# Kernel tuning notes

Hardware: AMD Instinct MI355X
Metric: run time of the kernel (lower is better)

Reference implementation:

```python
import jax, jax.numpy as jnp
import numpy as np

E, D, H, K = 8, 2048, 1024, 2  # num_experts, input_size, hidden_size, top_k
B, L = 2, 1024


def setup_inputs() -> dict:
    key = jax.random.key(0)
    k1, k2, k3, k4 = jax.random.split(key, 4)
    x = jax.random.normal(k1, (B, L, D), dtype=jnp.float32)
    w_gate = jax.random.normal(k2, (E, D), dtype=jnp.float32) * 0.02   # router Linear weight [E, D]
    w_in = jax.random.normal(k3, (E, 2 * H, D), dtype=jnp.float32) * 0.02  # ParallelExperts [E, out=2H, in=D]
    w_out = jax.random.normal(k4, (E, D, H), dtype=jnp.float32) * 0.02     # ParallelExperts [E, out=D, in=H]
    bias = jnp.zeros((D,), dtype=jnp.float32)
    return {"x": x, "w_gate": w_gate, "w_in": w_in, "w_out": w_out, "bias": bias}


def _moe_forward(x, w_gate, w_in, w_out, bias):
    bsz, length, d = x.shape
    xt = x.reshape(-1, d)  # [T, D]
    # top-k router: logits -> top-k -> softmax over selected logits
    logits = xt @ w_gate.T  # [T, E]
    topk_vals, topk_idx = jax.lax.top_k(logits, K)  # [T, K]
    topk_gates = jax.nn.softmax(topk_vals, axis=-1)  # [T, K]
    T = xt.shape[0]
    # dense [T, E] gate matrix; zero for non-selected experts, so the dense
    # per-expert compute below is mathematically identical to gathered dispatch
    gates = jnp.zeros((T, E), dtype=xt.dtype).at[jnp.arange(T)[:, None], topk_idx].add(topk_gates)
    # expert GLU FFN, vectorized over experts
    h = jnp.einsum('td,efd->tef', xt, w_in)  # [T, E, 2H]
    h1, h2 = jnp.split(h, 2, axis=-1)
    a = jax.nn.silu(h1) * h2                 # [T, E, H]
    eo = jnp.einsum('teh,edh->ted', a, w_out)  # [T, E, D]
    y = jnp.einsum('ted,te->td', eo, gates) + bias
    return y.reshape(bsz, length, d)


def reference(x, w_gate, w_in, w_out, bias):
    y = _moe_forward(x, w_gate, w_in, w_out, bias)
    loss = jnp.float32(0.0)  # router aux loss is 0 in eval mode (JetMoE top_k_gating)
    return (y, loss)
```

## Files before the change

### kernel.cpp

```cpp
#include <hip/hip_runtime.h>

#define E_    8
#define D_    2048
#define H_    1024
#define T_    2048
#define BK    64

using u16   = unsigned short;
using s16x8 = __attribute__((ext_vector_type(8))) short;
using f32x4 = __attribute__((ext_vector_type(4))) float;

__device__ __forceinline__ u16 f2bf(float f) {
  union { float f; unsigned u; } v; v.f = f;
  unsigned r = v.u + 0x7fffu + ((v.u >> 16) & 1u);
  return (u16)(r >> 16);
}
__device__ __forceinline__ s16x8 cvt8(f32x4 a, f32x4 b) {
  s16x8 o;
  o[0]=(short)f2bf(a.x); o[1]=(short)f2bf(a.y); o[2]=(short)f2bf(a.z); o[3]=(short)f2bf(a.w);
  o[4]=(short)f2bf(b.x); o[5]=(short)f2bf(b.y); o[6]=(short)f2bf(b.z); o[7]=(short)f2bf(b.w);
  return o;
}
__device__ __forceinline__ int slot(int r, int c) { return r * 64 + ((c ^ (r & 7)) << 3); }


__global__ __launch_bounds__(256) void init_kernel(
    const float* __restrict__ bias, float* __restrict__ out, int* __restrict__ counts)
{
  int idx = blockIdx.x * 256 + threadIdx.x;
  if (blockIdx.x == 0 && threadIdx.x < E_) counts[threadIdx.x] = 0;
  if (idx == 0) out[(size_t)T_ * D_] = 0.0f;
  int dq = idx & (D_ / 4 - 1);
  f32x4 b = *(const f32x4*)(bias + dq * 4);
  *(f32x4*)(out + (size_t)idx * 4) = b;
}

__global__ __launch_bounds__(256) void router_kernel(
    const float* __restrict__ x, const float* __restrict__ wg,
    u16* __restrict__ xb, int* __restrict__ lists, float* __restrict__ gates,
    int* __restrict__ counts)
{
  int t = blockIdx.x;
  int tid = threadIdx.x;
  const float* xr = x + (size_t)t * D_;
  float acc[E_];
#pragma unroll
  for (int e = 0; e < E_; ++e) acc[e] = 0.f;
#pragma unroll
  for (int i = 0; i < D_ / 256; ++i) {
    int d = tid + 256 * i;
    float xv = xr[d];
    xb[(size_t)t * D_ + d] = f2bf(xv);
#pragma unroll
    for (int e = 0; e < E_; ++e) acc[e] += xv * wg[e * D_ + d];
  }
#pragma unroll
  for (int off = 32; off >= 1; off >>= 1)
#pragma unroll
    for (int e = 0; e < E_; ++e) acc[e] += __shfl_down(acc[e], off);

  __shared__ float red[4][E_];
  int w = tid >> 6, lane = tid & 63;
  if (lane == 0)
#pragma unroll
    for (int e = 0; e < E_; ++e) red[w][e] = acc[e];
  __syncthreads();
  if (tid == 0) {
    float v0 = -1e30f, v1 = -1e30f; int e0 = 0, e1 = 0;
#pragma unroll
    for (int e = 0; e < E_; ++e) {
      float v = red[0][e] + red[1][e] + red[2][e] + red[3][e];
      if (v > v0)      { v1 = v0; e1 = e0; v0 = v; e0 = e; }
      else if (v > v1) { v1 = v;  e1 = e; }
    }
    float g1 = expf(v1 - v0);
    float inv = 1.f / (1.f + g1);
    float g0 = inv; g1 *= inv;
    int s0 = atomicAdd(&counts[e0], 1);
    lists[e0 * T_ + s0] = t * 2 + 0;
    gates[t * 2 + 0] = g0;
    int s1 = atomicAdd(&counts[e1], 1);
    lists[e1 * T_ + s1] = t * 2 + 1;
    gates[t * 2 + 1] = g1;
  }
}

__global__ __launch_bounds__(512) void gemm1_kernel(
    const u16* __restrict__ xb, const float* __restrict__ w_in,
    const int* __restrict__ lists, const int* __restrict__ counts,
    u16* __restrict__ a_buf)
{
  int e = blockIdx.z, bm = blockIdx.y, bn = blockIdx.x;
  int Ne = counts[e];
  if (bm * 256 >= Ne) return;

  __shared__ __align__(16) u16 As[2][256 * 64];
  __shared__ __align__(16) u16 Bs[2][128 * 64];

  int tid = threadIdx.x, w = tid >> 6, lane = tid & 63;
  int sr = tid >> 3, sc = tid & 7;
  int br = tid >> 2, bc = (tid & 3) * 2;

  const u16* aptr[4];
#pragma unroll
  for (int i = 0; i < 4; ++i) {
    int gr = bm * 256 + sr + 64 * i;
    aptr[i] = (gr < Ne) ? (xb + (size_t)(lists[e * T_ + gr] >> 1) * D_ + sc * 8) : nullptr;
  }
  int o = bn * 64 + ((br >> 5) & 1) * H_ + (br >> 6) * 32 + (br & 31);
  const float* bptr = w_in + (size_t)e * (2 * H_) * D_ + (size_t)o * D_ + bc * 8;

  s16x8 areg[4]; f32x4 bl[4];
#define LOADS1(K) { _Pragma("unroll") for (int i = 0; i < 4; ++i) { \
                      s16x8 v = {0,0,0,0,0,0,0,0}; \
                      if (aptr[i]) v = *(const s16x8*)(aptr[i] + (K)); areg[i] = v; } \
                    _Pragma("unroll") for (int i = 0; i < 4; ++i) \
                      bl[i] = *(const f32x4*)(bptr + (K) + i * 4); }
#define STAGE1(B) { _Pragma("unroll") for (int i = 0; i < 4; ++i) \
                      *(s16x8*)(&As[B][slot(sr + 64 * i, sc)]) = areg[i]; \
                    *(s16x8*)(&Bs[B][slot(br, bc)])     = cvt8(bl[0], bl[1]); \
                    *(s16x8*)(&Bs[B][slot(br, bc + 1)]) = cvt8(bl[2], bl[3]); }

  f32x4 acc[4][4];
#pragma unroll
  for (int m = 0; m < 4; ++m)
#pragma unroll
    for (int n = 0; n < 4; ++n) acc[m][n] = (f32x4){0.f, 0.f, 0.f, 0.f};

  int wr = (w >> 1) * 64, wc = (w & 1) * 64, lrow = lane & 15, g = lane >> 4;

  LOADS1(0);
  STAGE1(0);
  __syncthreads();
  const int NT = D_ / BK;
  for (int kt = 0; kt < NT; ++kt) {
    int cur = kt & 1;
    if (kt + 1 < NT) LOADS1((kt + 1) * BK);
#pragma unroll
    for (int ks = 0; ks < 2; ++ks) {
      int ch = ks * 4 + g;
      s16x8 af[4], bf[4];
#pragma unroll
      for (int m = 0; m < 4; ++m) af[m] = *(const s16x8*)(&As[cur][slot(wr + m * 16 + lrow, ch)]);
#pragma unroll
      for (int n = 0; n < 4; ++n) bf[n] = *(const s16x8*)(&Bs[cur][slot(wc + n * 16 + lrow, ch)]);
#pragma unroll
      for (int m = 0; m < 4; ++m)
#pragma unroll
        for (int n = 0; n < 4; ++n)
          acc[m][n] = __builtin_amdgcn_mfma_f32_16x16x32_bf16(af[m], bf[n], acc[m][n], 0, 0, 0);
    }
    if (kt + 1 < NT) {
      STAGE1(cur ^ 1);
      __syncthreads();
    }
  }
  int lcol = lane & 15, lr4 = (lane >> 4) * 4;
  int wcc = (w & 1) * 32;
#pragma unroll
  for (int m = 0; m < 4; ++m)
#pragma unroll
    for (int q = 0; q < 4; ++q) {
      int row = bm * 256 + wr + m * 16 + lr4 + q;
      if (row < Ne) {
#pragma unroll
        for (int n = 0; n < 2; ++n) {
          float h1 = acc[m][n][q], h2 = acc[m][n + 2][q];
          float a = (h1 / (1.f + __expf(-h1))) * h2;
          a_buf[((size_t)e * T_ + row) * H_ + bn * 64 + wcc + n * 16 + lcol] = f2bf(a);
        }
      }
    }
}

__global__ __launch_bounds__(512) void gemm2_kernel(
    const u16* __restrict__ a_buf, const float* __restrict__ w_out,
    const int* __restrict__ lists, const int* __restrict__ counts,
    const float* __restrict__ gates, float* __restrict__ out)
{
  int e = blockIdx.z, bm = blockIdx.y, bn = blockIdx.x;
  int Ne = counts[e];
  if (bm * 256 >= Ne) return;

  __shared__ __align__(16) u16 As[2][256 * 64];
  __shared__ __align__(16) u16 Bs[2][128 * 64];

  int tid = threadIdx.x, w = tid >> 6, lane = tid & 63;
  int sr = tid >> 3, sc = tid & 7;
  int br = tid >> 2, bc = (tid & 3) * 2;

  const u16* aptr[4];
#pragma unroll
  for (int i = 0; i < 4; ++i) {
    int gr = bm * 256 + sr + 64 * i;
    aptr[i] = (gr < Ne) ? (a_buf + ((size_t)e * T_ + gr) * H_ + sc * 8) : nullptr;
  }
  const float* bptr = w_out + (size_t)e * D_ * H_ + (size_t)(bn * 128 + br) * H_ + bc * 8;

  s16x8 areg[4]; f32x4 bl[4];
#define LOADS2(K) { _Pragma("unroll") for (int i = 0; i < 4; ++i) { \
                      s16x8 v = {0,0,0,0,0,0,0,0}; \
                      if (aptr[i]) v = *(const s16x8*)(aptr[i] + (K)); areg[i] = v; } \
                    _Pragma("unroll") for (int i = 0; i < 4; ++i) \
                      bl[i] = *(const f32x4*)(bptr + (K) + i * 4); }
#define STAGE2(B) { _Pragma("unroll") for (int i = 0; i < 4; ++i) \
                      *(s16x8*)(&As[B][slot(sr + 64 * i, sc)]) = areg[i]; \
                    *(s16x8*)(&Bs[B][slot(br, bc)])     = cvt8(bl[0], bl[1]); \
                    *(s16x8*)(&Bs[B][slot(br, bc + 1)]) = cvt8(bl[2], bl[3]); }

  f32x4 acc[4][4];
#pragma unroll
  for (int m = 0; m < 4; ++m)
#pragma unroll
    for (int n = 0; n < 4; ++n) acc[m][n] = (f32x4){0.f, 0.f, 0.f, 0.f};

  int wr = (w >> 1) * 64, wc = (w & 1) * 64, lrow = lane & 15, g = lane >> 4;

  LOADS2(0);
  STAGE2(0);
  __syncthreads();
  const int NT = H_ / BK;
  for (int kt = 0; kt < NT; ++kt) {
    int cur = kt & 1;
    if (kt + 1 < NT) LOADS2((kt + 1) * BK);
#pragma unroll
    for (int ks = 0; ks < 2; ++ks) {
      int ch = ks * 4 + g;
      s16x8 af[4], bf[4];
#pragma unroll
      for (int m = 0; m < 4; ++m) af[m] = *(const s16x8*)(&As[cur][slot(wr + m * 16 + lrow, ch)]);
#pragma unroll
      for (int n = 0; n < 4; ++n) bf[n] = *(const s16x8*)(&Bs[cur][slot(wc + n * 16 + lrow, ch)]);
#pragma unroll
      for (int m = 0; m < 4; ++m)
#pragma unroll
        for (int n = 0; n < 4; ++n)
          acc[m][n] = __builtin_amdgcn_mfma_f32_16x16x32_bf16(af[m], bf[n], acc[m][n], 0, 0, 0);
    }
    if (kt + 1 < NT) {
      STAGE2(cur ^ 1);
      __syncthreads();
    }
  }
  int lcol = lane & 15, lr4 = (lane >> 4) * 4;
#pragma unroll
  for (int m = 0; m < 4; ++m)
#pragma unroll
    for (int q = 0; q < 4; ++q) {
      int row = bm * 256 + wr + m * 16 + lr4 + q;
      if (row < Ne) {
        int p = lists[e * T_ + row];
        float gt = gates[p];
        int t = p >> 1;
#pragma unroll
        for (int n = 0; n < 4; ++n)
          atomicAdd(&out[(size_t)t * D_ + bn * 128 + wc + n * 16 + lcol], gt * acc[m][n][q]);
      }
    }
}

extern "C" void kernel_launch(void* const* d_in, const int* in_sizes, int n_in,
                              void* d_out, int out_size, void* d_ws, size_t ws_size,
                              hipStream_t stream)
{
  const float* x      = (const float*)d_in[0];
  const float* w_gate = (const float*)d_in[1];
  const float* w_in   = (const float*)d_in[2];
  const float* w_out  = (const float*)d_in[3];
  const float* bias   = (const float*)d_in[4];
  float* out = (float*)d_out;

  char* ws = (char*)d_ws;
  u16*   xb     = (u16*)(ws);
  u16*   a_buf  = (u16*)(ws + 8388608);
  int*   lists  = (int*)(ws + 41943040);
  float* gates  = (float*)(ws + 42008576);
  int*   counts = (int*)(ws + 42024960);

  init_kernel<<<T_ * D_ / 4 / 256, 256, 0, stream>>>(bias, out, counts);
  router_kernel<<<T_, 256, 0, stream>>>(x, w_gate, xb, lists, gates, counts);
  dim3 g1(H_ / 64, 8, E_);
  gemm1_kernel<<<g1, 512, 0, stream>>>(xb, w_in, lists, counts, a_buf);
  dim3 g2(D_ / 128, 8, E_);
  gemm2_kernel<<<g2, 512, 0, stream>>>(a_buf, w_out, lists, counts, gates, out);
}
```

Before: 232.5 us.

## Use persistent grid-stride tile scheduling with narrower N tiles and direct-to-LDS loads

Both grouped GEMMs now launch a fixed grid of 512 blocks. Each block walks a flattened list of (expert M-tile, N-tile) work items through a prefix scan over per-expert counts, so no blocks launch only to exit early. The N tile is halved to 64 and occupancy is hinted at 4 blocks per CU. Activation tiles go straight into LDS via global_load_lds with a pre-swizzled column, replacing the register staging. Narrower tiles cut per-tile reuse of the gathered activations and double the number of tiles, and out-of-range rows are now clamped to the last valid row instead of zeroed.

```diff
diff --git a/kernel.cpp b/kernel.cpp
--- a/kernel.cpp
+++ b/kernel.cpp
@@ -5,6 +5,7 @@
 #define H_    1024
 #define T_    2048
 #define BK    64
+#define NN    32
 
 using u16   = unsigned short;
 using s16x8 = __attribute__((ext_vector_type(8))) short;
@@ -22,6 +23,20 @@
   return o;
 }
 __device__ __forceinline__ int slot(int r, int c) { return r * 64 + ((c ^ (r & 7)) << 3); }
+
+__device__ __forceinline__ void gload16(const void* g, void* l) {
+  __builtin_amdgcn_global_load_lds((const __attribute__((address_space(1))) void*)g,
+                                   (__attribute__((address_space(3))) void*)l, 16, 0, 0);
+}
+
+#define FIND_EXPERT(ml, cnt, e, mt, Ne)                        \
+  { int b_ = 0;                                                \
+    _Pragma("unroll")                                          \
+    for (int i_ = 0; i_ < E_; ++i_) {                          \
+      int ti_ = (cnt[i_] + 255) >> 8;                          \
+      if ((ml) >= b_ && (ml) < b_ + ti_) {                     \
+        e = i_; mt = (ml) - b_; Ne = cnt[i_]; }                \
+      b_ += ti_; } }
 
 
 __global__ __launch_bounds__(256) void init_kernel(
@@ -85,178 +100,186 @@
   }
 }
 
-__global__ __launch_bounds__(512) void gemm1_kernel(
+__global__ __launch_bounds__(512, 4) void gemm1_kernel(
     const u16* __restrict__ xb, const float* __restrict__ w_in,
     const int* __restrict__ lists, const int* __restrict__ counts,
     u16* __restrict__ a_buf)
 {
-  int e = blockIdx.z, bm = blockIdx.y, bn = blockIdx.x;
-  int Ne = counts[e];
-  if (bm * 256 >= Ne) return;
-
   __shared__ __align__(16) u16 As[2][256 * 64];
-  __shared__ __align__(16) u16 Bs[2][128 * 64];
+  __shared__ __align__(16) u16 Bs[2][64 * 64];
+
+  int cnt[E_];
+#pragma unroll
+  for (int i = 0; i < E_; ++i) cnt[i] = counts[i];
+  int mt_total = 0;
+#pragma unroll
+  for (int i = 0; i < E_; ++i) mt_total += (cnt[i] + 255) >> 8;
+  int total = mt_total * NN;
 
   int tid = threadIdx.x, w = tid >> 6, lane = tid & 63;
-  int sr = tid >> 3, sc = tid & 7;
-  int br = tid >> 2, bc = (tid & 3) * 2;
-
-  const u16* aptr[4];
-#pragma unroll
-  for (int i = 0; i < 4; ++i) {
-    int gr = bm * 256 + sr + 64 * i;
-    aptr[i] = (gr < Ne) ? (xb + (size_t)(lists[e * T_ + gr] >> 1) * D_ + sc * 8) : nullptr;
+  int swzc = ((lane & 7) ^ (lane >> 3)) * 8;
+  int brow = tid >> 3, bch = tid & 7;
+  int wr = (w >> 1) * 64, wcB = (w & 1) * 32, lrow = lane & 15, g = lane >> 4;
+  int lcol = lane & 15, lr4 = (lane >> 4) * 4;
+
+  int bswz = (blockIdx.x & 7) * 64 + (blockIdx.x >> 3);
+
+  for (int t = bswz; t < total; t += 512) {
+    int ml = t >> 5, n = t & (NN - 1);
+    int e = 0, mt = 0, Ne = 0;
+    FIND_EXPERT(ml, cnt, e, mt, Ne);
+
+    const u16* ap[4];
+#pragma unroll
+    for (int i = 0; i < 4; ++i) {
+      int gr = mt * 256 + 32 * w + 8 * i + (lane >> 3);
+      if (gr >= Ne) gr = Ne - 1;
+      ap[i] = xb + (size_t)(lists[e * T_ + gr] >> 1) * D_ + swzc;
+    }
+    int o = n * 32 + ((brow >> 4) & 1) * H_ + (brow >> 5) * 16 + (brow & 15);
+    const float* bp = w_in + (size_t)e * (2 * H_) * D_ + (size_t)o * D_ + bch * 8;
+
+    f32x4 acc[4][2];
+#pragma unroll
+    for (int m = 0; m < 4; ++m) { acc[m][0] = (f32x4){0,0,0,0}; acc[m][1] = (f32x4){0,0,0,0}; }
+
+    f32x4 bl0 = *(const f32x4*)(bp), bl1 = *(const f32x4*)(bp + 4);
+#pragma unroll
+    for (int i = 0; i < 4; ++i) gload16(ap[i], &As[0][(32 * w + 8 * i) * 64]);
+    *(s16x8*)(&Bs[0][slot(brow, bch)]) = cvt8(bl0, bl1);
+    __syncthreads();
+
+    const int NT = D_ / BK;
+    for (int kt = 0; kt < NT; ++kt) {
+      int cur = kt & 1;
+      if (kt + 1 < NT) {
+        int k = (kt + 1) * BK;
+        bl0 = *(const f32x4*)(bp + k); bl1 = *(const f32x4*)(bp + k + 4);
+#pragma unroll
+        for (int i = 0; i < 4; ++i) gload16(ap[i] + k, &As[cur ^ 1][(32 * w + 8 * i) * 64]);
+      }
+#pragma unroll
+      for (int ks = 0; ks < 2; ++ks) {
+        int ch = ks * 4 + g;
+        s16x8 af[4], bf[2];
+#pragma unroll
+        for (int m = 0; m < 4; ++m) af[m] = *(const s16x8*)(&As[cur][slot(wr + m * 16 + lrow, ch)]);
+#pragma unroll
+        for (int nn = 0; nn < 2; ++nn) bf[nn] = *(const s16x8*)(&Bs[cur][slot(wcB + nn * 16 + lrow, ch)]);
+#pragma unroll
+        for (int m = 0; m < 4; ++m)
+#pragma unroll
+          for (int nn = 0; nn < 2; ++nn)
+            acc[m][nn] = __builtin_amdgcn_mfma_f32_16x16x32_bf16(af[m], bf[nn], acc[m][nn], 0, 0, 0);
+      }
+      if (kt + 1 < NT)
+        *(s16x8*)(&Bs[cur ^ 1][slot(brow, bch)]) = cvt8(bl0, bl1);
+      __syncthreads();
+    }
+#pragma unroll
+    for (int m = 0; m < 4; ++m)
+#pragma unroll
+      for (int q = 0; q < 4; ++q) {
+        int row = mt * 256 + wr + m * 16 + lr4 + q;
+        if (row < Ne) {
+          float h1 = acc[m][0][q], h2 = acc[m][1][q];
+          float a = (h1 / (1.f + __expf(-h1))) * h2;
+          a_buf[((size_t)e * T_ + row) * H_ + n * 32 + (w & 1) * 16 + lcol] = f2bf(a);
+        }
+      }
   }
-  int o = bn * 64 + ((br >> 5) & 1) * H_ + (br >> 6) * 32 + (br & 31);
-  const float* bptr = w_in + (size_t)e * (2 * H_) * D_ + (size_t)o * D_ + bc * 8;
-
-  s16x8 areg[4]; f32x4 bl[4];
-#define LOADS1(K) { _Pragma("unroll") for (int i = 0; i < 4; ++i) { \
-                      s16x8 v = {0,0,0,0,0,0,0,0}; \
-                      if (aptr[i]) v = *(const s16x8*)(aptr[i] + (K)); areg[i] = v; } \
-                    _Pragma("unroll") for (int i = 0; i < 4; ++i) \
-                      bl[i] = *(const f32x4*)(bptr + (K) + i * 4); }
-#define STAGE1(B) { _Pragma("unroll") for (int i = 0; i < 4; ++i) \
-                      *(s16x8*)(&As[B][slot(sr + 64 * i, sc)]) = areg[i]; \
-                    *(s16x8*)(&Bs[B][slot(br, bc)])     = cvt8(bl[0], bl[1]); \
-                    *(s16x8*)(&Bs[B][slot(br, bc + 1)]) = cvt8(bl[2], bl[3]); }
-
-  f32x4 acc[4][4];
-#pragma unroll
-  for (int m = 0; m < 4; ++m)
-#pragma unroll
-    for (int n = 0; n < 4; ++n) acc[m][n] = (f32x4){0.f, 0.f, 0.f, 0.f};
-
-  int wr = (w >> 1) * 64, wc = (w & 1) * 64, lrow = lane & 15, g = lane >> 4;
-
-  LOADS1(0);
-  STAGE1(0);
-  __syncthreads();
-  const int NT = D_ / BK;
-  for (int kt = 0; kt < NT; ++kt) {
-    int cur = kt & 1;
-    if (kt + 1 < NT) LOADS1((kt + 1) * BK);
-#pragma unroll
-    for (int ks = 0; ks < 2; ++ks) {
-      int ch = ks * 4 + g;
-      s16x8 af[4], bf[4];
-#pragma unroll
-      for (int m = 0; m < 4; ++m) af[m] = *(const s16x8*)(&As[cur][slot(wr + m * 16 + lrow, ch)]);
-#pragma unroll
-      for (int n = 0; n < 4; ++n) bf[n] = *(const s16x8*)(&Bs[cur][slot(wc + n * 16 + lrow, ch)]);
-#pragma unroll
-      for (int m = 0; m < 4; ++m)
-#pragma unroll
-        for (int n = 0; n < 4; ++n)
-          acc[m][n] = __builtin_amdgcn_mfma_f32_16x16x32_bf16(af[m], bf[n], acc[m][n], 0, 0, 0);
-    }
-    if (kt + 1 < NT) {
-      STAGE1(cur ^ 1);
-      __syncthreads();
-    }
-  }
-  int lcol = lane & 15, lr4 = (lane >> 4) * 4;
-  int wcc = (w & 1) * 32;
-#pragma unroll
-  for (int m = 0; m < 4; ++m)
-#pragma unroll
-    for (int q = 0; q < 4; ++q) {
-      int row = bm * 256 + wr + m * 16 + lr4 + q;
-      if (row < Ne) {
-#pragma unroll
-        for (int n = 0; n < 2; ++n) {
-          float h1 = acc[m][n][q], h2 = acc[m][n + 2][q];
-          float a = (h1 / (1.f + __expf(-h1))) * h2;
-          a_buf[((size_t)e * T_ + row) * H_ + bn * 64 + wcc + n * 16 + lcol] = f2bf(a);
-        }
-      }
-    }
-}
-
-__global__ __launch_bounds__(512) void gemm2_kernel(
+}
+
+__global__ __launch_bounds__(512, 4) void gemm2_kernel(
     const u16* __restrict__ a_buf, const float* __restrict__ w_out,
     const int* __restrict__ lists, const int* __restrict__ counts,
     const float* __restrict__ gates, float* __restrict__ out)
 {
-  int e = blockIdx.z, bm = blockIdx.y, bn = blockIdx.x;
-  int Ne = counts[e];
-  if (bm * 256 >= Ne) return;
-
   __shared__ __align__(16) u16 As[2][256 * 64];
-  __shared__ __align__(16) u16 Bs[2][128 * 64];
+  __shared__ __align__(16) u16 Bs[2][64 * 64];
+
+  int cnt[E_];
+#pragma unroll
+  for (int i = 0; i < E_; ++i) cnt[i] = counts[i];
+  int mt_total = 0;
+#pragma unroll
+  for (int i = 0; i < E_; ++i) mt_total += (cnt[i] + 255) >> 8;
+  int total = mt_total * NN;
 
   int tid = threadIdx.x, w = tid >> 6, lane = tid & 63;
-  int sr = tid >> 3, sc = tid & 7;
-  int br = tid >> 2, bc = (tid & 3) * 2;
-
-  const u16* aptr[4];
-#pragma unroll
-  for (int i = 0; i < 4; ++i) {
-    int gr = bm * 256 + sr + 64 * i;
-    aptr[i] = (gr < Ne) ? (a_buf + ((size_t)e * T_ + gr) * H_ + sc * 8) : nullptr;
+  int swzc = ((lane & 7) ^ (lane >> 3)) * 8;
+  int brow = tid >> 3, bch = tid & 7;
+  int wr = (w >> 1) * 64, wcB = (w & 1) * 32, lrow = lane & 15, g = lane >> 4;
+  int lcol = lane & 15, lr4 = (lane >> 4) * 4;
+
+  int bswz = (blockIdx.x & 7) * 64 + (blockIdx.x >> 3);
+
+  for (int t = bswz; t < total; t += 512) {
+    int ml = t >> 5, n = t & (NN - 1);
+    int e = 0, mt = 0, Ne = 0;
+    FIND_EXPERT(ml, cnt, e, mt, Ne);
+
+    const u16* ap[4];
+#pragma unroll
+    for (int i = 0; i < 4; ++i) {
+      int gr = mt * 256 + 32 * w + 8 * i + (lane >> 3);
+      if (gr >= Ne) gr = Ne - 1;
+      ap[i] = a_buf + ((size_t)e * T_ + gr) * H_ + swzc;
+    }
+    const float* bp = w_out + (size_t)e * D_ * H_ + (size_t)(n * 64 + brow) * H_ + bch * 8;
+
+    f32x4 acc[4][2];
+#pragma unroll
+    for (int m = 0; m < 4; ++m) { acc[m][0] = (f32x4){0,0,0,0}; acc[m][1] = (f32x4){0,0,0,0}; }
+
+    f32x4 bl0 = *(const f32x4*)(bp), bl1 = *(const f32x4*)(bp + 4);
+#pragma unroll
+    for (int i = 0; i < 4; ++i) gload16(ap[i], &As[0][(32 * w + 8 * i) * 64]);
+    *(s16x8*)(&Bs[0][slot(brow, bch)]) = cvt8(bl0, bl1);
+    __syncthreads();
+
+    const int NT = H_ / BK;
+    for (int kt = 0; kt < NT; ++kt) {
+      int cur = kt & 1;
+      if (kt + 1 < NT) {
+        int k = (kt + 1) * BK;
+        bl0 = *(const f32x4*)(bp + k); bl1 = *(const f32x4*)(bp + k + 4);
+#pragma unroll
+        for (int i = 0; i < 4; ++i) gload16(ap[i] + k, &As[cur ^ 1][(32 * w + 8 * i) * 64]);
+      }
+#pragma unroll
+      for (int ks = 0; ks < 2; ++ks) {
+        int ch = ks * 4 + g;
+        s16x8 af[4], bf[2];
+#pragma unroll
+        for (int m = 0; m < 4; ++m) af[m] = *(const s16x8*)(&As[cur][slot(wr + m * 16 + lrow, ch)]);
+#pragma unroll
+        for (int nn = 0; nn < 2; ++nn) bf[nn] = *(const s16x8*)(&Bs[cur][slot(wcB + nn * 16 + lrow, ch)]);
+#pragma unroll
+        for (int m = 0; m < 4; ++m)
+#pragma unroll
+          for (int nn = 0; nn < 2; ++nn)
+            acc[m][nn] = __builtin_amdgcn_mfma_f32_16x16x32_bf16(af[m], bf[nn], acc[m][nn], 0, 0, 0);
+      }
+      if (kt + 1 < NT)
+        *(s16x8*)(&Bs[cur ^ 1][slot(brow, bch)]) = cvt8(bl0, bl1);
+      __syncthreads();
+    }
+#pragma unroll
+    for (int m = 0; m < 4; ++m)
+#pragma unroll
+      for (int q = 0; q < 4; ++q) {
+        int row = mt * 256 + wr + m * 16 + lr4 + q;
+        if (row < Ne) {
+          int p = lists[e * T_ + row];
+          float gt = gates[p];
+          int tok = p >> 1;
+#pragma unroll
+          for (int nn = 0; nn < 2; ++nn)
+            atomicAdd(&out[(size_t)tok * D_ + n * 64 + wcB + nn * 16 + lcol], gt * acc[m][nn][q]);
+        }
+      }
   }
-  const float* bptr = w_out + (size_t)e * D_ * H_ + (size_t)(bn * 128 + br) * H_ + bc * 8;
-
-  s16x8 areg[4]; f32x4 bl[4];
-#define LOADS2(K) { _Pragma("unroll") for (int i = 0; i < 4; ++i) { \
-                      s16x8 v = {0,0,0,0,0,0,0,0}; \
-                      if (aptr[i]) v = *(const s16x8*)(aptr[i] + (K)); areg[i] = v; } \
-                    _Pragma("unroll") for (int i = 0; i < 4; ++i) \
-                      bl[i] = *(const f32x4*)(bptr + (K) + i * 4); }
-#define STAGE2(B) { _Pragma("unroll") for (int i = 0; i < 4; ++i) \
-                      *(s16x8*)(&As[B][slot(sr + 64 * i, sc)]) = areg[i]; \
-                    *(s16x8*)(&Bs[B][slot(br, bc)])     = cvt8(bl[0], bl[1]); \
-                    *(s16x8*)(&Bs[B][slot(br, bc + 1)]) = cvt8(bl[2], bl[3]); }
-
-  f32x4 acc[4][4];
-#pragma unroll
-  for (int m = 0; m < 4; ++m)
-#pragma unroll
-    for (int n = 0; n < 4; ++n) acc[m][n] = (f32x4){0.f, 0.f, 0.f, 0.f};
-
-  int wr = (w >> 1) * 64, wc = (w & 1) * 64, lrow = lane & 15, g = lane >> 4;
-
-  LOADS2(0);
-  STAGE2(0);
-  __syncthreads();
-  const int NT = H_ / BK;
-  for (int kt = 0; kt < NT; ++kt) {
-    int cur = kt & 1;
-    if (kt + 1 < NT) LOADS2((kt + 1) * BK);
-#pragma unroll
-    for (int ks = 0; ks < 2; ++ks) {
-      int ch = ks * 4 + g;
-      s16x8 af[4], bf[4];
-#pragma unroll
-      for (int m = 0; m < 4; ++m) af[m] = *(const s16x8*)(&As[cur][slot(wr + m * 16 + lrow, ch)]);
-#pragma unroll
-      for (int n = 0; n < 4; ++n) bf[n] = *(const s16x8*)(&Bs[cur][slot(wc + n * 16 + lrow, ch)]);
-#pragma unroll
-      for (int m = 0; m < 4; ++m)
-#pragma unroll
-        for (int n = 0; n < 4; ++n)
-          acc[m][n] = __builtin_amdgcn_mfma_f32_16x16x32_bf16(af[m], bf[n], acc[m][n], 0, 0, 0);
-    }
-    if (kt + 1 < NT) {
-      STAGE2(cur ^ 1);
-      __syncthreads();
-    }
-  }
-  int lcol = lane & 15, lr4 = (lane >> 4) * 4;
-#pragma unroll
-  for (int m = 0; m < 4; ++m)
-#pragma unroll
-    for (int q = 0; q < 4; ++q) {
-      int row = bm * 256 + wr + m * 16 + lr4 + q;
-      if (row < Ne) {
-        int p = lists[e * T_ + row];
-        float gt = gates[p];
-        int t = p >> 1;
-#pragma unroll
-        for (int n = 0; n < 4; ++n)
-          atomicAdd(&out[(size_t)t * D_ + bn * 128 + wc + n * 16 + lcol], gt * acc[m][n][q]);
-      }
-    }
 }
 
 extern "C" void kernel_launch(void* const* d_in, const int* in_sizes, int n_in,
@@ -279,8 +302,6 @@
 
   init_kernel<<<T_ * D_ / 4 / 256, 256, 0, stream>>>(bias, out, counts);
   router_kernel<<<T_, 256, 0, stream>>>(x, w_gate, xb, lists, gates, counts);
-  dim3 g1(H_ / 64, 8, E_);
-  gemm1_kernel<<<g1, 512, 0, stream>>>(xb, w_in, lists, counts, a_buf);
-  dim3 g2(D_ / 128, 8, E_);
-  gemm2_kernel<<<g2, 512, 0, stream>>>(a_buf, w_out, lists, counts, gates, out);
-}
+  gemm1_kernel<<<512, 512, 0, stream>>>(xb, w_in, lists, counts, a_buf);
+  gemm2_kernel<<<512, 512, 0, stream>>>(a_buf, w_out, lists, counts, gates, out);
+}
```

New measurement: 244.6 us. 1.05x slower.
